# Kernel tuning notes

Hardware: AMD Instinct MI355X
Metric: run time of the kernel (lower is better)

The kernel has to match this reference:

```python
import jax, jax.numpy as jnp
import numpy as np

B, S, HID, NH = 4, 2048, 2048, 16
HD = HID // NH
DECAY_INIT = 0.95


def setup_inputs() -> dict:
    key = jax.random.key(0)
    k1, k2, k3 = jax.random.split(key, 3)
    x = jax.random.normal(k1, (B, S, HID), jnp.float32)
    # torch Linear weights stored as [in, out] for x @ W; scaled like default init
    W_qkv = jax.random.normal(k2, (HID, 3 * HID), jnp.float32) / np.float32(np.sqrt(HID))
    W_out = jax.random.normal(k3, (HID, HID), jnp.float32) / np.float32(np.sqrt(HID))
    decay_param = jnp.full((NH,), DECAY_INIT, jnp.float32)
    kv0 = jnp.zeros((B, NH, HD), jnp.float32)
    k_sum0 = jnp.zeros((B, NH, HD), jnp.float32)
    attention_mask = jnp.ones((B, 1, 1, S), jnp.float32)
    return dict(x=x, kv0=kv0, k_sum0=k_sum0, attention_mask=attention_mask,
                W_qkv=W_qkv, W_out=W_out, decay_param=decay_param)


def _phi(u):
    # kernel feature map: elu(x) + 1 (non-negative)
    return jax.nn.elu(u) + 1.0


def reference(x, kv0, k_sum0, attention_mask, W_qkv, W_out, decay_param):
    b, s, hid = x.shape
    nh = decay_param.shape[0]
    hd = hid // nh
    qkv = x @ W_qkv                               # [b, s, 3*hid]
    q, k, v = jnp.split(qkv, 3, axis=-1)

    def to_time_major(t):                         # [b, s, hid] -> [s, b, nh, hd]
        return t.reshape(b, s, nh, hd).transpose(1, 0, 2, 3)

    q = _phi(to_time_major(q))
    k = _phi(to_time_major(k))
    v = to_time_major(v)

    # mask [b,1,1,s] -> [s, b, 1, 1]; padded tokens don't update the state
    m = attention_mask.reshape(b, 1, s, 1).transpose(2, 0, 1, 3)
    k = k * m
    v = v * m

    decay = jax.nn.sigmoid(decay_param)[None, :, None]  # [1, nh, 1]

    def step(carry, inp):
        kv, ks = carry                             # each [b, nh, hd]
        q_t, k_t, v_t = inp                        # each [b, nh, hd]
        kv = decay * kv + k_t * v_t
        ks = decay * ks + k_t
        num = jnp.sum(q_t * kv, axis=-1, keepdims=True)
        den = jnp.maximum(jnp.sum(q_t * ks, axis=-1, keepdims=True), 1e-6)
        return (kv, ks), (num / den) * q_t

    (kv, ks), outs = jax.lax.scan(step, (kv0, k_sum0), (q, k, v))
    out = outs.transpose(1, 0, 2, 3).reshape(b, s, hid) @ W_out
    return out, kv, ks
```

## Files before the change

### kernel.cpp

```cpp
#include <hip/hip_runtime.h>
#include <hip/hip_bf16.h>

typedef __hip_bfloat16 bf16;
typedef short bf16x8 __attribute__((ext_vector_type(8)));
typedef float f32x4 __attribute__((ext_vector_type(4)));

#define BB   4
#define SS   2048
#define HID  2048
#define NHD  16
#define HD   128
#define NCH  64
#define CHL  32

__device__ inline float b2f(bf16 v) { return __bfloat162float(v); }
__device__ inline float sigm(float x) { return 1.f / (1.f + __expf(-x)); }
__device__ inline float phi_f(float v) { return v > 0.f ? v + 1.f : __expf(v); }

__device__ inline int probe_fp32(const void* probe) {
    return ((const unsigned*)probe)[0] != 0x3F733F73u;
}
__device__ inline float ldd(const void* p, int fp32, size_t i) {
    return fp32 ? ((const float*)p)[i] : __bfloat162float(((const bf16*)p)[i]);
}
__device__ inline void st_dual(void* p, int fp32, size_t i, float v) {
    if (fp32) ((float*)p)[i] = v;
    else      ((bf16*)p)[i] = __float2bfloat16(v);
}

__device__ inline void ld2(const bf16* p, float& a, float& b) {
    unsigned u = *(const unsigned*)p;
    union U { unsigned x; float f; } lo, hi;
    lo.x = u << 16; hi.x = u & 0xffff0000u;
    a = lo.f; b = hi.f;
}
__device__ inline void st2(bf16* p, float a, float b) {
    __hip_bfloat162 v;
    v.x = __float2bfloat16(a);
    v.y = __float2bfloat16(b);
    *(__hip_bfloat162*)p = v;
}

__device__ __forceinline__ void gload_lds16(const bf16* g, bf16* l) {
    __builtin_amdgcn_global_load_lds((const __attribute__((address_space(1))) void*)g,
                                     (__attribute__((address_space(3))) void*)l,
                                     16, 0, 0);
}

__global__ __launch_bounds__(256) void cvt_bf16(const void* __restrict__ in,
                                                bf16* __restrict__ out,
                                                const void* __restrict__ probe,
                                                size_t n) {
    int fp32 = probe_fp32(probe);
    size_t i = ((size_t)blockIdx.x * 256 + threadIdx.x) * 4;
    if (i >= n) return;
    if (fp32) {
        float4 v = *(const float4*)((const float*)in + i);
        bf16* o = out + i;
        o[0] = __float2bfloat16(v.x); o[1] = __float2bfloat16(v.y);
        o[2] = __float2bfloat16(v.z); o[3] = __float2bfloat16(v.w);
    } else {
        *(short4*)(out + i) = *(const short4*)((const bf16*)in + i);
    }
}

__global__ __launch_bounds__(256) void transpose_any(const void* __restrict__ in,
                                                     bf16* __restrict__ out,
                                                     const void* __restrict__ probe,
                                                     int R, int C) {
    int fp32 = probe_fp32(probe);
    __shared__ bf16 t[64][65];
    int c0 = blockIdx.x * 64;
    int r0 = blockIdx.y * 64;
    int tid = threadIdx.x;
    int c = tid & 63;
    int rb = tid >> 6;
#pragma unroll
    for (int i = 0; i < 16; i++) {
        int r = rb + i * 4;
        t[r][c] = __float2bfloat16(ldd(in, fp32, (size_t)(r0 + r) * C + c0 + c));
    }
    __syncthreads();
#pragma unroll
    for (int i = 0; i < 16; i++) {
        int r = rb + i * 4;
        out[(size_t)(c0 + r) * R + r0 + c] = t[c][r];
    }
}

template <int EPI>
__global__ __launch_bounds__(256) void gemm_bt(const bf16* __restrict__ A,
                                               const bf16* __restrict__ Bt,
                                               void* __restrict__ Cv,
                                               const void* __restrict__ mask,
                                               const void* __restrict__ probe,
                                               int M, int N, int K) {
    int fp32 = probe_fp32(probe);
    __shared__ __align__(16) short lA[128 * 32];
    __shared__ __align__(16) short lB[128 * 32];
    int tid = threadIdx.x;
    int lane = tid & 63, wave = tid >> 6;
    int quad = lane >> 4, l15 = lane & 15;
    int wm = (wave >> 1) * 64, wn = (wave & 1) * 64;
    int m0 = blockIdx.y * 128, n0 = blockIdx.x * 128;

    int srow_l = lane >> 2;
    int gq     = (lane & 3) ^ ((lane >> 3) & 3);
    int cA0 = 2 * wave, cA1 = 2 * wave + 1;
    const bf16* gA0 = A  + (size_t)(m0 + cA0 * 16 + srow_l) * K + gq * 8;
    const bf16* gA1 = A  + (size_t)(m0 + cA1 * 16 + srow_l) * K + gq * 8;
    const bf16* gB0 = Bt + (size_t)(n0 + cA0 * 16 + srow_l) * K + gq * 8;
    const bf16* gB1 = Bt + (size_t)(n0 + cA1 * 16 + srow_l) * K + gq * 8;
    bf16* lA0 = (bf16*)&lA[cA0 * 512];
    bf16* lA1 = (bf16*)&lA[cA1 * 512];
    bf16* lB0 = (bf16*)&lB[cA0 * 512];
    bf16* lB1 = (bf16*)&lB[cA1 * 512];

    int sq = quad ^ ((l15 >> 1) & 3);

    f32x4 zero = {0.f, 0.f, 0.f, 0.f};
    f32x4 acc[4][4];
#pragma unroll
    for (int i = 0; i < 4; i++)
#pragma unroll
        for (int j = 0; j < 4; j++) acc[i][j] = zero;

    for (int kt = 0; kt < K; kt += 32) {
        __syncthreads();
        gload_lds16(gA0 + kt, lA0);
        gload_lds16(gA1 + kt, lA1);
        gload_lds16(gB0 + kt, lB0);
        gload_lds16(gB1 + kt, lB1);
        __syncthreads();

        bf16x8 af[4], bfr[4];
#pragma unroll
        for (int i = 0; i < 4; i++)
            af[i] = *(const bf16x8*)&lA[(wm + i * 16 + l15) * 32 + sq * 8];
#pragma unroll
        for (int j = 0; j < 4; j++)
            bfr[j] = *(const bf16x8*)&lB[(wn + j * 16 + l15) * 32 + sq * 8];
#pragma unroll
        for (int i = 0; i < 4; i++)
#pragma unroll
            for (int j = 0; j < 4; j++)
                acc[i][j] = __builtin_amdgcn_mfma_f32_16x16x32_bf16(af[i], bfr[j],
                                                                    acc[i][j], 0, 0, 0);
    }

#pragma unroll
    for (int i = 0; i < 4; i++) {
#pragma unroll
        for (int r = 0; r < 4; r++) {
            int m = m0 + wm + i * 16 + quad * 4 + r;
            float mk = 1.f;
            if (EPI) mk = ldd(mask, fp32, m);
#pragma unroll
            for (int j = 0; j < 4; j++) {
                int n = n0 + wn + j * 16 + l15;
                float v = acc[i][j][r];
                if (EPI) {
                    if (n < HID)            v = phi_f(v);
                    else if (n < 2 * HID)   v = phi_f(v) * mk;
                    else                    v = v * mk;
                    ((bf16*)Cv)[(size_t)m * N + n] = __float2bfloat16(v);
                } else {
                    st_dual(Cv, fp32, (size_t)m * N + n, v);
                }
            }
        }
    }
}

__global__ __launch_bounds__(64) void scan_local(const bf16* __restrict__ qkv,
                                                 float* __restrict__ ckv,
                                                 float* __restrict__ cks,
                                                 const void* __restrict__ decp) {
    int fp32 = probe_fp32(decp);
    int blk = blockIdx.x;
    int bh = blk / NCH, c = blk % NCH;
    int b = bh >> 4, h = bh & 15;
    int lane = threadIdx.x;
    int hd = lane * 2;
    float dec = sigm(ldd(decp, fp32, h));
    const bf16* kb = qkv + (size_t)(b * SS + c * CHL) * (3 * HID) + HID + h * HD + hd;
    const bf16* vb = kb + HID;
    float kv0 = 0.f, kv1 = 0.f, ks0 = 0.f, ks1 = 0.f;
    for (int t = 0; t < CHL; t++) {
        float k0, k1, v0, v1;
        ld2(kb, k0, k1);
        ld2(vb, v0, v1);
        kb += 3 * HID; vb += 3 * HID;
        kv0 = dec * kv0 + k0 * v0;
        kv1 = dec * kv1 + k1 * v1;
        ks0 = dec * ks0 + k0;
        ks1 = dec * ks1 + k1;
    }
    int o = blk * HD + hd;
    ckv[o] = kv0; ckv[o + 1] = kv1;
    cks[o] = ks0; cks[o + 1] = ks1;
}

__global__ __launch_bounds__(128) void scan_combine(const float* __restrict__ ckv,
                                                    const float* __restrict__ cks,
                                                    const void* __restrict__ kv0in,
                                                    const void* __restrict__ ks0in,
                                                    const void* __restrict__ decp,
                                                    float* __restrict__ ikv,
                                                    float* __restrict__ iks,
                                                    void* __restrict__ outbase) {
    int fp32 = probe_fp32(decp);
    int bh = blockIdx.x;
    int h = bh & 15;
    int hd = threadIdx.x;
    float dec = sigm(ldd(decp, fp32, h));
    float dl = powf(dec, (float)CHL);
    float skv = ldd(kv0in, fp32, bh * HD + hd);
    float sks = ldd(ks0in, fp32, bh * HD + hd);
    for (int c = 0; c < NCH; c++) {
        int o = (bh * NCH + c) * HD + hd;
        ikv[o] = skv; iks[o] = sks;
        skv = dl * skv + ckv[o];
        sks = dl * sks + cks[o];
    }
    size_t base = (size_t)BB * SS * HID;
    st_dual(outbase, fp32, base + bh * HD + hd, skv);
    st_dual(outbase, fp32, base + BB * NHD * HD + bh * HD + hd, sks);
}

__global__ __launch_bounds__(64) void scan_out(const bf16* __restrict__ qkv,
                                               const float* __restrict__ ikv,
                                               const float* __restrict__ iks,
                                               const void* __restrict__ decp,
                                               bf16* __restrict__ outs) {
    int fp32 = probe_fp32(decp);
    int blk = blockIdx.x;
    int bh = blk / NCH, c = blk % NCH;
    int b = bh >> 4, h = bh & 15;
    int lane = threadIdx.x;
    int hd = lane * 2;
    float dec = sigm(ldd(decp, fp32, h));
    int o = blk * HD + hd;
    float kva = ikv[o], kvb = ikv[o + 1];
    float ksa = iks[o], ksb = iks[o + 1];
    const bf16* qb = qkv + (size_t)(b * SS + c * CHL) * (3 * HID) + h * HD + hd;
    const bf16* kb = qb + HID;
    const bf16* vb = qb + 2 * HID;
    bf16* ob = outs + (size_t)(b * SS + c * CHL) * HID + h * HD + hd;
    for (int t = 0; t < CHL; t++) {
        float q0, q1, k0, k1, v0, v1;
        ld2(qb, q0, q1);
        ld2(kb, k0, k1);
        ld2(vb, v0, v1);
        qb += 3 * HID; kb += 3 * HID; vb += 3 * HID;
        kva = dec * kva + k0 * v0;
        kvb = dec * kvb + k1 * v1;
        ksa = dec * ksa + k0;
        ksb = dec * ksb + k1;
        float num = q0 * kva + q1 * kvb;
        float den = q0 * ksa + q1 * ksb;
#pragma unroll
        for (int off = 32; off > 0; off >>= 1) {
            num += __shfl_xor(num, off);
            den += __shfl_xor(den, off);
        }
        float sc = num / fmaxf(den, 1e-6f);
        st2(ob, q0 * sc, q1 * sc);
        ob += HID;
    }
}

extern "C" void kernel_launch(void* const* d_in, const int* in_sizes, int n_in,
                              void* d_out, int out_size, void* d_ws, size_t ws_size,
                              hipStream_t stream) {
    const void* x    = d_in[0];
    const void* kv0  = d_in[1];
    const void* ks0  = d_in[2];
    const void* am   = d_in[3];
    const void* Wqkv = d_in[4];
    const void* Wout = d_in[5];
    const void* decp = d_in[6];

    const int M = BB * SS;
    const int N1 = 3 * HID;
    const int K = HID;

    char* ws = (char*)d_ws;
    bf16* WqkvT = (bf16*)ws;  ws += (size_t)N1 * K * 2;
    bf16* WoutT = (bf16*)ws;  ws += (size_t)HID * HID * 2;
    bf16* x_bf  = (bf16*)ws;  ws += (size_t)M * HID * 2;
    bf16* qkvb  = (bf16*)ws;  ws += (size_t)M * N1 * 2;
    bf16* outs  = (bf16*)ws;  ws += (size_t)M * HID * 2;
    float* ckv  = (float*)ws; ws += (size_t)BB * NHD * NCH * HD * 4;
    float* cks  = (float*)ws; ws += (size_t)BB * NHD * NCH * HD * 4;
    float* ikv  = (float*)ws; ws += (size_t)BB * NHD * NCH * HD * 4;
    float* iks  = (float*)ws; ws += (size_t)BB * NHD * NCH * HD * 4;

    cvt_bf16<<<(size_t)M * HID / 4 / 256, 256, 0, stream>>>(x, x_bf, decp, (size_t)M * HID);
    transpose_any<<<dim3(N1 / 64, K / 64), 256, 0, stream>>>(Wqkv, WqkvT, decp, K, N1);
    transpose_any<<<dim3(HID / 64, HID / 64), 256, 0, stream>>>(Wout, WoutT, decp, K, HID);

    gemm_bt<1><<<dim3(N1 / 128, M / 128), 256, 0, stream>>>(x_bf, WqkvT, qkvb, am, decp,
                                                            M, N1, K);

    scan_local<<<BB * NHD * NCH, 64, 0, stream>>>(qkvb, ckv, cks, decp);
    scan_combine<<<BB * NHD, 128, 0, stream>>>(ckv, cks, kv0, ks0, decp, ikv, iks, d_out);
    scan_out<<<BB * NHD * NCH, 64, 0, stream>>>(qkvb, ikv, iks, decp, outs);

    gemm_bt<0><<<dim3(HID / 128, M / 128), 256, 0, stream>>>(outs, WoutT, d_out, nullptr,
                                                             decp, M, HID, K);
}
```

Baseline: 606.9 us.

## Fuse prep kernels, widen GEMM K-tile to 64, fold scan combine into scan_out

Merges the bf16 conversion of x and the two weight transposes into one prep launch. Doubles the GEMM K tile from 32 to 64 with a new XOR swizzle, halving the barriers per K. Removes the scan_combine kernel: each scan_out block rebuilds its starting state by a serial prefix over earlier chunk summaries, and the last chunk writes the final state. This saves two launches and intermediate buffers, but adds redundant prefix work that grows with chunk index and doubles GEMM LDS use.

```diff
diff --git a/kernel.cpp b/kernel.cpp
--- a/kernel.cpp
+++ b/kernel.cpp
@@ -13,7 +13,6 @@
 #define NCH  64
 #define CHL  32
 
-__device__ inline float b2f(bf16 v) { return __bfloat162float(v); }
 __device__ inline float sigm(float x) { return 1.f / (1.f + __expf(-x)); }
 __device__ inline float phi_f(float v) { return v > 0.f ? v + 1.f : __expf(v); }
 
@@ -47,32 +46,41 @@
                                      16, 0, 0);
 }
 
-__global__ __launch_bounds__(256) void cvt_bf16(const void* __restrict__ in,
-                                                bf16* __restrict__ out,
-                                                const void* __restrict__ probe,
-                                                size_t n) {
+#define NB_CVT 16384
+#define NB_T1  3072
+#define NB_T2  1024
+__global__ __launch_bounds__(256) void prep(const void* __restrict__ x,
+                                            bf16* __restrict__ x_bf,
+                                            const void* __restrict__ Wqkv,
+                                            bf16* __restrict__ WqkvT,
+                                            const void* __restrict__ Wout,
+                                            bf16* __restrict__ WoutT,
+                                            const void* __restrict__ probe) {
     int fp32 = probe_fp32(probe);
-    size_t i = ((size_t)blockIdx.x * 256 + threadIdx.x) * 4;
-    if (i >= n) return;
-    if (fp32) {
-        float4 v = *(const float4*)((const float*)in + i);
-        bf16* o = out + i;
-        o[0] = __float2bfloat16(v.x); o[1] = __float2bfloat16(v.y);
-        o[2] = __float2bfloat16(v.z); o[3] = __float2bfloat16(v.w);
+    int bid = blockIdx.x;
+    int tid = threadIdx.x;
+    if (bid < NB_CVT) {
+        size_t i = ((size_t)bid * 256 + tid) * 4;
+        if (fp32) {
+            float4 v = *(const float4*)((const float*)x + i);
+            bf16* o = x_bf + i;
+            o[0] = __float2bfloat16(v.x); o[1] = __float2bfloat16(v.y);
+            o[2] = __float2bfloat16(v.z); o[3] = __float2bfloat16(v.w);
+        } else {
+            *(short4*)(x_bf + i) = *(const short4*)((const bf16*)x + i);
+        }
+        return;
+    }
+    const void* in; bf16* out; int R, C, idx;
+    if (bid < NB_CVT + NB_T1) {
+        in = Wqkv; out = WqkvT; R = HID; C = 3 * HID; idx = bid - NB_CVT;
     } else {
-        *(short4*)(out + i) = *(const short4*)((const bf16*)in + i);
-    }
-}
-
-__global__ __launch_bounds__(256) void transpose_any(const void* __restrict__ in,
-                                                     bf16* __restrict__ out,
-                                                     const void* __restrict__ probe,
-                                                     int R, int C) {
-    int fp32 = probe_fp32(probe);
+        in = Wout; out = WoutT; R = HID; C = HID; idx = bid - NB_CVT - NB_T1;
+    }
+    int ctiles = C / 64;
+    int c0 = (idx % ctiles) * 64;
+    int r0 = (idx / ctiles) * 64;
     __shared__ bf16 t[64][65];
-    int c0 = blockIdx.x * 64;
-    int r0 = blockIdx.y * 64;
-    int tid = threadIdx.x;
     int c = tid & 63;
     int rb = tid >> 6;
 #pragma unroll
@@ -96,27 +104,23 @@
                                                const void* __restrict__ probe,
                                                int M, int N, int K) {
     int fp32 = probe_fp32(probe);
-    __shared__ __align__(16) short lA[128 * 32];
-    __shared__ __align__(16) short lB[128 * 32];
+    __shared__ __align__(16) short lA[128 * 64];
+    __shared__ __align__(16) short lB[128 * 64];
     int tid = threadIdx.x;
     int lane = tid & 63, wave = tid >> 6;
     int quad = lane >> 4, l15 = lane & 15;
     int wm = (wave >> 1) * 64, wn = (wave & 1) * 64;
     int m0 = blockIdx.y * 128, n0 = blockIdx.x * 128;
 
-    int srow_l = lane >> 2;
-    int gq     = (lane & 3) ^ ((lane >> 3) & 3);
-    int cA0 = 2 * wave, cA1 = 2 * wave + 1;
-    const bf16* gA0 = A  + (size_t)(m0 + cA0 * 16 + srow_l) * K + gq * 8;
-    const bf16* gA1 = A  + (size_t)(m0 + cA1 * 16 + srow_l) * K + gq * 8;
-    const bf16* gB0 = Bt + (size_t)(n0 + cA0 * 16 + srow_l) * K + gq * 8;
-    const bf16* gB1 = Bt + (size_t)(n0 + cA1 * 16 + srow_l) * K + gq * 8;
-    bf16* lA0 = (bf16*)&lA[cA0 * 512];
-    bf16* lA1 = (bf16*)&lA[cA1 * 512];
-    bf16* lB0 = (bf16*)&lB[cA0 * 512];
-    bf16* lB1 = (bf16*)&lB[cA1 * 512];
-
-    int sq = quad ^ ((l15 >> 1) & 3);
+    int r8 = lane >> 3;
+    int pu = lane & 7;
+    int gu = pu ^ r8;
+    const bf16* gA = A  + (size_t)(m0 + wave * 32 + r8) * K + gu * 8;
+    const bf16* gB = Bt + (size_t)(n0 + wave * 32 + r8) * K + gu * 8;
+    bf16* lAw = (bf16*)&lA[(wave * 32) * 64];
+    bf16* lBw = (bf16*)&lB[(wave * 32) * 64];
+
+    int sw = l15 & 7;
 
     f32x4 zero = {0.f, 0.f, 0.f, 0.f};
     f32x4 acc[4][4];
@@ -125,27 +129,33 @@
 #pragma unroll
         for (int j = 0; j < 4; j++) acc[i][j] = zero;
 
-    for (int kt = 0; kt < K; kt += 32) {
+    for (int kt = 0; kt < K; kt += 64) {
         __syncthreads();
-        gload_lds16(gA0 + kt, lA0);
-        gload_lds16(gA1 + kt, lA1);
-        gload_lds16(gB0 + kt, lB0);
-        gload_lds16(gB1 + kt, lB1);
+#pragma unroll
+        for (int g = 0; g < 4; g++) {
+            gload_lds16(gA + kt + (size_t)g * 8 * K, lAw + g * 512);
+            gload_lds16(gB + kt + (size_t)g * 8 * K, lBw + g * 512);
+        }
         __syncthreads();
 
-        bf16x8 af[4], bfr[4];
-#pragma unroll
-        for (int i = 0; i < 4; i++)
-            af[i] = *(const bf16x8*)&lA[(wm + i * 16 + l15) * 32 + sq * 8];
-#pragma unroll
-        for (int j = 0; j < 4; j++)
-            bfr[j] = *(const bf16x8*)&lB[(wn + j * 16 + l15) * 32 + sq * 8];
-#pragma unroll
-        for (int i = 0; i < 4; i++)
+#pragma unroll
+        for (int s = 0; s < 2; s++) {
+            bf16x8 af[4], bfr[4];
+#pragma unroll
+            for (int i = 0; i < 4; i++)
+                af[i] = *(const bf16x8*)&lA[(wm + i * 16 + l15) * 64 +
+                                            ((quad + 4 * s) ^ sw) * 8];
 #pragma unroll
             for (int j = 0; j < 4; j++)
-                acc[i][j] = __builtin_amdgcn_mfma_f32_16x16x32_bf16(af[i], bfr[j],
-                                                                    acc[i][j], 0, 0, 0);
+                bfr[j] = *(const bf16x8*)&lB[(wn + j * 16 + l15) * 64 +
+                                             ((quad + 4 * s) ^ sw) * 8];
+#pragma unroll
+            for (int i = 0; i < 4; i++)
+#pragma unroll
+                for (int j = 0; j < 4; j++)
+                    acc[i][j] = __builtin_amdgcn_mfma_f32_16x16x32_bf16(af[i], bfr[j],
+                                                                        acc[i][j], 0, 0, 0);
+        }
     }
 
 #pragma unroll
@@ -201,38 +211,14 @@
     cks[o] = ks0; cks[o + 1] = ks1;
 }
 
-__global__ __launch_bounds__(128) void scan_combine(const float* __restrict__ ckv,
-                                                    const float* __restrict__ cks,
-                                                    const void* __restrict__ kv0in,
-                                                    const void* __restrict__ ks0in,
-                                                    const void* __restrict__ decp,
-                                                    float* __restrict__ ikv,
-                                                    float* __restrict__ iks,
-                                                    void* __restrict__ outbase) {
-    int fp32 = probe_fp32(decp);
-    int bh = blockIdx.x;
-    int h = bh & 15;
-    int hd = threadIdx.x;
-    float dec = sigm(ldd(decp, fp32, h));
-    float dl = powf(dec, (float)CHL);
-    float skv = ldd(kv0in, fp32, bh * HD + hd);
-    float sks = ldd(ks0in, fp32, bh * HD + hd);
-    for (int c = 0; c < NCH; c++) {
-        int o = (bh * NCH + c) * HD + hd;
-        ikv[o] = skv; iks[o] = sks;
-        skv = dl * skv + ckv[o];
-        sks = dl * sks + cks[o];
-    }
-    size_t base = (size_t)BB * SS * HID;
-    st_dual(outbase, fp32, base + bh * HD + hd, skv);
-    st_dual(outbase, fp32, base + BB * NHD * HD + bh * HD + hd, sks);
-}
-
 __global__ __launch_bounds__(64) void scan_out(const bf16* __restrict__ qkv,
-                                               const float* __restrict__ ikv,
-                                               const float* __restrict__ iks,
+                                               const float* __restrict__ ckv,
+                                               const float* __restrict__ cks,
+                                               const void* __restrict__ kv0in,
+                                               const void* __restrict__ ks0in,
                                                const void* __restrict__ decp,
-                                               bf16* __restrict__ outs) {
+                                               bf16* __restrict__ outs,
+                                               void* __restrict__ outbase) {
     int fp32 = probe_fp32(decp);
     int blk = blockIdx.x;
     int bh = blk / NCH, c = blk % NCH;
@@ -240,9 +226,20 @@
     int lane = threadIdx.x;
     int hd = lane * 2;
     float dec = sigm(ldd(decp, fp32, h));
-    int o = blk * HD + hd;
-    float kva = ikv[o], kvb = ikv[o + 1];
-    float ksa = iks[o], ksb = iks[o + 1];
+    float dl = powf(dec, (float)CHL);
+
+    float kva = ldd(kv0in, fp32, bh * HD + hd);
+    float kvb = ldd(kv0in, fp32, bh * HD + hd + 1);
+    float ksa = ldd(ks0in, fp32, bh * HD + hd);
+    float ksb = ldd(ks0in, fp32, bh * HD + hd + 1);
+    for (int j = 0; j < c; j++) {
+        int o = (bh * NCH + j) * HD + hd;
+        kva = dl * kva + ckv[o];
+        kvb = dl * kvb + ckv[o + 1];
+        ksa = dl * ksa + cks[o];
+        ksb = dl * ksb + cks[o + 1];
+    }
+
     const bf16* qb = qkv + (size_t)(b * SS + c * CHL) * (3 * HID) + h * HD + hd;
     const bf16* kb = qb + HID;
     const bf16* vb = qb + 2 * HID;
@@ -268,6 +265,14 @@
         st2(ob, q0 * sc, q1 * sc);
         ob += HID;
     }
+
+    if (c == NCH - 1) {
+        size_t base = (size_t)BB * SS * HID;
+        st_dual(outbase, fp32, base + bh * HD + hd, kva);
+        st_dual(outbase, fp32, base + bh * HD + hd + 1, kvb);
+        st_dual(outbase, fp32, base + BB * NHD * HD + bh * HD + hd, ksa);
+        st_dual(outbase, fp32, base + BB * NHD * HD + bh * HD + hd + 1, ksb);
+    }
 }
 
 extern "C" void kernel_launch(void* const* d_in, const int* in_sizes, int n_in,
@@ -293,19 +298,16 @@
     bf16* outs  = (bf16*)ws;  ws += (size_t)M * HID * 2;
     float* ckv  = (float*)ws; ws += (size_t)BB * NHD * NCH * HD * 4;
     float* cks  = (float*)ws; ws += (size_t)BB * NHD * NCH * HD * 4;
-    float* ikv  = (float*)ws; ws += (size_t)BB * NHD * NCH * HD * 4;
-    float* iks  = (float*)ws; ws += (size_t)BB * NHD * NCH * HD * 4;
-
-    cvt_bf16<<<(size_t)M * HID / 4 / 256, 256, 0, stream>>>(x, x_bf, decp, (size_t)M * HID);
-    transpose_any<<<dim3(N1 / 64, K / 64), 256, 0, stream>>>(Wqkv, WqkvT, decp, K, N1);
-    transpose_any<<<dim3(HID / 64, HID / 64), 256, 0, stream>>>(Wout, WoutT, decp, K, HID);
+
+    prep<<<NB_CVT + NB_T1 + NB_T2, 256, 0, stream>>>(x, x_bf, Wqkv, WqkvT,
+                                                     Wout, WoutT, decp);
 
     gemm_bt<1><<<dim3(N1 / 128, M / 128), 256, 0, stream>>>(x_bf, WqkvT, qkvb, am, decp,
                                                             M, N1, K);
 
     scan_local<<<BB * NHD * NCH, 64, 0, stream>>>(qkvb, ckv, cks, decp);
-    scan_combine<<<BB * NHD, 128, 0, stream>>>(ckv, cks, kv0, ks0, decp, ikv, iks, d_out);
-    scan_out<<<BB * NHD * NCH, 64, 0, stream>>>(qkvb, ikv, iks, decp, outs);
+    scan_out<<<BB * NHD * NCH, 64, 0, stream>>>(qkvb, ckv, cks, kv0, ks0, decp,
+                                                outs, d_out);
 
     gemm_bt<0><<<dim3(HID / 128, M / 128), 256, 0, stream>>>(outs, WoutT, d_out, nullptr,
                                                              decp, M, HID, K);
```

After: 562.3 us. 7.3% less time.
